# Kernel tuning notes

Hardware: AMD Instinct MI355X
Metric: run time of the kernel (lower is better)

## Reference

```python
import jax, jax.numpy as jnp
import numpy as np

# 27 kernel taps x 3 offset components (dz, dy, dx), matching the module's offset0 list.
OFFSET0 = np.array([
    1, 1, 1, 1, 1, 0, 1, 1, -1, 1, 0, 1, 1, 0, 0, 1, 0, -1, 1, -1, 1, 1, -1, 0, 1, -1, -1,
    0, 1, 1, 0, 1, 0, 0, 1, -1, 0, 0, 1, 0, 0, 0, 0, 0, -1, 0, -1, 1, 0, -1, 0, 0, -1, -1,
    -1, 1, 1, -1, 1, 0, -1, 1, -1, -1, 0, 1, -1, 0, 0, -1, 0, -1, -1, -1, 1, -1, -1, 0, -1, -1, -1
], dtype=np.float64).reshape(27, 3)

BN_EPS = 1e-5


def upsample_nearest2(x):
    # nn.Upsample(scale_factor=2), default mode='nearest', on [B,C,Z,Y,X]
    x = jnp.repeat(x, 2, axis=2)
    x = jnp.repeat(x, 2, axis=3)
    return jnp.repeat(x, 2, axis=4)


def deform_conv3d_static(x, W, b, alpha):
    """3D deformable conv, kernel 3, pad 1, stride 1, with spatially-constant
    per-tap offsets alpha*OFFSET0. Zero padding outside; trilinear sampling.
    Since offsets are static, each tap samples at a fixed fractional shift,
    implemented as a static trilinear combination of slices of the padded input.
    x: [B,C,Z,Y,X], W: [O,C,3,3,3], b: [O].
    """
    B, C, Z, Y, X = x.shape
    # pad 2: 1 for the 3x3x3 kernel + 1 for fractional offsets (|alpha*d| <= 0.7)
    xp = jnp.pad(x, ((0, 0), (0, 0), (2, 2), (2, 2), (2, 2)))
    out = None
    t = 0
    for kz in range(3):
        for ky in range(3):
            for kx in range(3):
                dz, dy, dx = (alpha * OFFSET0[t]).tolist()
                s = (kz - 1 + dz, ky - 1 + dy, kx - 1 + dx)  # shift rel. to output voxel
                f = [int(np.floor(v)) for v in s]
                w = [v - fl for v, fl in zip(s, f)]
                vol = None
                for cz in (0, 1):
                    for cy in (0, 1):
                        for cx in (0, 1):
                            wt = ((w[0] if cz else 1.0 - w[0]) *
                                  (w[1] if cy else 1.0 - w[1]) *
                                  (w[2] if cx else 1.0 - w[2]))
                            if wt == 0.0:
                                continue
                            z0 = 2 + f[0] + cz
                            y0 = 2 + f[1] + cy
                            x0 = 2 + f[2] + cx
                            sl = xp[:, :, z0:z0 + Z, y0:y0 + Y, x0:x0 + X]
                            sl = jnp.float32(wt) * sl
                            vol = sl if vol is None else vol + sl
                contrib = jnp.einsum('oc,bczyx->bozyx', W[:, :, kz, ky, kx], vol)
                out = contrib if out is None else out + contrib
                t += 1
    return out + b[None, :, None, None, None]


def batchnorm(x, g, bt, m, v):
    # eval-mode BatchNorm3d over channel axis 1
    inv = g * jax.lax.rsqrt(v + BN_EPS)
    return x * inv[None, :, None, None, None] + (bt - m * inv)[None, :, None, None, None]


def setup_inputs() -> dict:
    key = jax.random.key(0)
    ks = jax.random.split(key, 13)
    ch_in, ch_out = 64, 32
    x = jax.random.normal(ks[0], (1, ch_in, 32, 32, 32), jnp.float32)
    w_def = jax.random.normal(ks[1], (ch_out, ch_in, 3, 3, 3), jnp.float32) * 0.05
    b_def = jax.random.normal(ks[2], (ch_out,), jnp.float32) * 0.05
    bn1_g = 1.0 + 0.1 * jax.random.normal(ks[3], (ch_out,), jnp.float32)
    bn1_b = 0.1 * jax.random.normal(ks[4], (ch_out,), jnp.float32)
    bn1_m = 0.1 * jax.random.normal(ks[5], (ch_out,), jnp.float32)
    bn1_v = jax.random.uniform(ks[6], (ch_out,), jnp.float32, 0.5, 1.5)
    w_comb = jax.random.normal(ks[7], (ch_out, 3 * ch_out), jnp.float32) * 0.1
    b_comb = 0.05 * jax.random.normal(ks[8], (ch_out,), jnp.float32)
    bn2_g = 1.0 + 0.1 * jax.random.normal(ks[9], (ch_out,), jnp.float32)
    bn2_b = 0.1 * jax.random.normal(ks[10], (ch_out,), jnp.float32)
    bn2_m = 0.1 * jax.random.normal(ks[11], (ch_out,), jnp.float32)
    bn2_v = jax.random.uniform(ks[12], (ch_out,), jnp.float32, 0.5, 1.5)
    return {"x": x, "w_def": w_def, "b_def": b_def,
            "bn1_g": bn1_g, "bn1_b": bn1_b, "bn1_m": bn1_m, "bn1_v": bn1_v,
            "w_comb": w_comb, "b_comb": b_comb,
            "bn2_g": bn2_g, "bn2_b": bn2_b, "bn2_m": bn2_m, "bn2_v": bn2_v}


def reference(x, w_def, b_def, bn1_g, bn1_b, bn1_m, bn1_v,
              w_comb, b_comb, bn2_g, bn2_b, bn2_m, bn2_v):
    xu = upsample_nearest2(x)
    branches = []
    for alpha in (0.0, 0.4, 0.7):  # shared deform-conv weights, three static offset scales
        o = deform_conv3d_static(xu, w_def, b_def, alpha)
        o = jax.nn.relu(batchnorm(o, bn1_g, bn1_b, bn1_m, bn1_v))
        branches.append(o)
    cat = jnp.concatenate(branches, axis=1)  # [B, 3*ch_out, Z,Y,X]
    y = jnp.einsum('oc,bczyx->bozyx', w_comb, cat) + b_comb[None, :, None, None, None]
    y = batchnorm(y, bn2_g, bn2_b, bn2_m, bn2_v)
    return jax.nn.relu(y)
```

## Files before the change

kernel.cpp:

```cpp
#include <hip/hip_runtime.h>


typedef __bf16 bf16x8 __attribute__((ext_vector_type(8)));
typedef float f32x16 __attribute__((ext_vector_type(16)));
typedef unsigned u32x2 __attribute__((ext_vector_type(2)));

__device__ inline unsigned short f2bf(float f) {
  unsigned int u = __float_as_uint(f);
  u += 0x7FFFu + ((u >> 16) & 1u);
  return (unsigned short)(u >> 16);
}

__device__ inline bf16x8 bc16(uint4 v) { return __builtin_bit_cast(bf16x8, v); }

__device__ inline unsigned cvtpk(float lo, float hi) {
  unsigned r;
  asm("v_cvt_pk_bf16_f32 %0, %1, %2" : "=v"(r) : "v"(lo), "v"(hi));
  return r;
}

__device__ inline void plswap(unsigned& a, unsigned& b) {
  u32x2 r = __builtin_amdgcn_permlane32_swap(a, b, false, false);
  a = r.x;
  b = r.y;
}

__device__ inline void gload16(const unsigned short* g, unsigned short* l) {
  __builtin_amdgcn_global_load_lds(
      (const __attribute__((address_space(1))) unsigned int*)(const void*)g,
      (__attribute__((address_space(3))) unsigned int*)(void*)l, 16, 0, 0);
}

__device__ inline float ucoef(int abit, int k, int jbit, float alpha) {
  if (abit == 0) return (k == 0) ? (jbit ? alpha : 1.f - alpha) : (jbit ? 1.f : 0.f);
  return (k == 2) ? (jbit ? 1.f - alpha : alpha) : (jbit ? 0.f : 1.f);
}

#define XREG_USH 524352
#define XZERO_B 1048576u

__global__ void k_prep(const float* __restrict__ x, unsigned short* __restrict__ xT2,
                       const float* __restrict__ w_def, const float* __restrict__ bn1_g,
                       const float* __restrict__ bn1_v, unsigned short* __restrict__ W_sw,
                       const float* __restrict__ w_comb, const float* __restrict__ b_comb,
                       const float* __restrict__ bn2_g, const float* __restrict__ bn2_b,
                       const float* __restrict__ bn2_m, const float* __restrict__ bn2_v,
                       const float* __restrict__ b_def, const float* __restrict__ bn1_b,
                       const float* __restrict__ bn1_m, unsigned short* __restrict__ W2_sw,
                       float* __restrict__ bias1, float* __restrict__ bias2) {
  __shared__ unsigned short t[64][65];
  int bid = blockIdx.x;
  if (bid < 512) {
    int s0 = bid * 64;
    int lane = threadIdx.x & 63;
    int grp = threadIdx.x >> 6;
#pragma unroll
    for (int c = grp; c < 64; c += 4)
      t[c][lane] = f2bf(x[c * 32768 + s0 + lane]);
    __syncthreads();
    int q = lane >> 4, e = lane & 15;
#pragma unroll
    for (int s = grp; s < 64; s += 4)
      xT2[q * XREG_USH + (size_t)(s0 + s) * 16 + e] = t[lane][s];
  } else if (bid < 2048) {
    int e = (bid - 512) * 256 + threadIdx.x;
    int j = e & 7;
    int lane = (e >> 3) & 63;
    int idx = e >> 9;
    int nt = idx % 3;
    idx /= 3;
    int s = idx & 31;
    int p = idx >> 5;
    int o = lane & 31;
    int br = nt;
    int kk = 16 * s + ((lane >> 5) << 3) + j;
    int tap = kk >> 6, ch = kk & 63;
    int jz = (tap >> 2) & 1, jy = (tap >> 1) & 1, jx = tap & 1;
    int a = (p >> 2) & 1, b = (p >> 1) & 1, cp = p & 1;
    float alpha = (br == 0) ? 0.f : ((br == 1) ? 0.4f : 0.7f);
    const float* wb = w_def + (o * 64 + ch) * 27;
    float sum = 0.f;
    for (int kz = 0; kz < 3; ++kz) {
      float uz = ucoef(a, kz, jz, alpha);
      if (uz == 0.f) continue;
      for (int ky = 0; ky < 3; ++ky) {
        float uy = ucoef(b, ky, jy, alpha);
        if (uy == 0.f) continue;
        float uzy = uz * uy;
        for (int kx = 0; kx < 3; ++kx) {
          float ux = ucoef(cp, kx, jx, alpha);
          if (ux != 0.f) sum += wb[kz * 9 + ky * 3 + kx] * uzy * ux;
        }
      }
    }
    float s1 = bn1_g[o] * rsqrtf(bn1_v[o] + 1e-5f);
    W_sw[e] = f2bf(sum * s1);
  } else {
    int tid = threadIdx.x;
    for (int e = tid; e < 3072; e += 256) {
      int j = e & 7;
      int lane = (e >> 3) & 63;
      int s2 = e >> 9;
      int n = lane & 31;
      int k = 16 * s2 + ((lane >> 5) << 3) + j;
      float sc2 = bn2_g[n] * rsqrtf(bn2_v[n] + 1e-5f);
      W2_sw[e] = f2bf(w_comb[n * 96 + k] * sc2);
    }
    {
      int q = tid >> 6, e2 = tid & 63;
      xT2[q * XREG_USH + 524288 + e2] = 0;
    }
    if (tid < 32) {
      float s1 = bn1_g[tid] * rsqrtf(bn1_v[tid] + 1e-5f);
      bias1[tid] = (b_def[tid] - bn1_m[tid]) * s1 + bn1_b[tid];
      float s2 = bn2_g[tid] * rsqrtf(bn2_v[tid] + 1e-5f);
      bias2[tid] = (b_comb[tid] - bn2_m[tid]) * s2 + bn2_b[tid];
    }
  }
}

__launch_bounds__(256, 2)
__global__ void k_main(const unsigned short* __restrict__ xT2,
                       const unsigned short* __restrict__ W_sw,
                       const unsigned short* __restrict__ W2_sw,
                       const float* __restrict__ bias1f,
                       const float* __restrict__ bias2f,
                       float* __restrict__ out) {
  __shared__ unsigned short wring[2][12288];
  __shared__ float blds[64];
  int tid = threadIdx.x;
  int lane = tid & 63;
  int wv = tid >> 6;
  int bid = blockIdx.x;
  int tb = (bid & 7) | ((bid >> 5) << 3);
  int ph = (bid >> 3) & 3;
  int bph = ph & 1, a = ph >> 1;
  int tx = tb & 3, ty = (tb >> 2) & 3, tz = tb >> 4;
  int i0 = tz * 4, j0 = ty * 8, k0 = tx * 8;

  if (tid < 32) {
    blds[tid] = bias1f[tid];
    blds[32 + tid] = bias2f[tid];
  }

  int h = lane >> 5;
  int m = lane & 31;
  int ax = m & 7, ay = (m >> 3) & 1, az = m >> 4;
  int p0 = (a << 2) | (bph << 1);
  unsigned hb = (unsigned)(h << 4);

  const char* xq0 = (const char*)xT2;
  const char* xq1 = xq0 + 1048704;
  const char* xq2 = xq0 + 2097408;
  const char* xq3 = xq0 + 3146112;

  auto stage = [&](int cc) {
    int pn = p0 | (cc >> 2);
    const unsigned short* g =
        W_sw + pn * 49152 + (cc & 3) * 12288 + wv * 3072 + lane * 8;
    unsigned short* l = &wring[cc & 1][wv * 3072];
#pragma unroll
    for (int k = 0; k < 6; ++k) gload16(g + k * 512, l + k * 512);
  };

  __syncthreads();
  stage(0);

  f32x16 osv0, osv1;
  f32x16 acc[2][3];
#pragma unroll
  for (int mt = 0; mt < 2; ++mt)
#pragma unroll
    for (int nt = 0; nt < 3; ++nt) acc[mt][nt] = (f32x16)0.f;

  for (int cc = 0; cc < 8; ++cc) {
    asm volatile("s_waitcnt vmcnt(0)" ::: "memory");
    __builtin_amdgcn_s_barrier();
    __builtin_amdgcn_sched_barrier(0);
    if (cc < 7) stage(cc + 1);
    __builtin_amdgcn_sched_barrier(0);

    int cp = cc >> 2, jy = cc & 1, jz = (cc >> 1) & 1;
    int gz0i = i0 + a - 1 + az + jz;
    int gz1i = gz0i + 2;
    int gyi = j0 + bph - 1 + 2 * wv + ay + jy;
    int gx0i = k0 - 1 + ax + cp;
    int gx1i = gx0i + 1;
    bool oky = (unsigned)gyi < 32u;
    bool okz0 = (unsigned)gz0i < 32u, okz1 = (unsigned)gz1i < 32u;
    bool okx0 = (unsigned)gx0i < 32u, okx1 = (unsigned)gx1i < 32u;
    unsigned s00 = (unsigned)(((gz0i * 32 + gyi) * 32 + gx0i) * 32) + hb;
    unsigned s01 = (unsigned)(((gz1i * 32 + gyi) * 32 + gx0i) * 32) + hb;
    unsigned s10 = (unsigned)(((gz0i * 32 + gyi) * 32 + gx1i) * 32) + hb;
    unsigned s11 = (unsigned)(((gz1i * 32 + gyi) * 32 + gx1i) * 32) + hb;
    unsigned v00 = (oky && okz0 && okx0) ? s00 : XZERO_B;
    unsigned v01 = (oky && okz1 && okx0) ? s01 : XZERO_B;
    unsigned v10 = (oky && okz0 && okx1) ? s10 : XZERO_B;
    unsigned v11 = (oky && okz1 && okx1) ? s11 : XZERO_B;

    const unsigned short* wfb = &wring[cc & 1][lane * 8];
#pragma unroll
    for (int tl = 0; tl < 2; ++tl) {
      unsigned va0 = tl ? v10 : v00;
      unsigned va1 = tl ? v11 : v01;
#pragma unroll
      for (int q = 0; q < 4; ++q) {
        const char* xb = (q == 0) ? xq0 : (q == 1) ? xq1 : (q == 2) ? xq2 : xq3;
        bf16x8 a0 = bc16(*(const uint4*)(xb + va0));
        bf16x8 a1 = bc16(*(const uint4*)(xb + va1));
        const unsigned short* wf = wfb + tl * 6144 + q * 1536;
        bf16x8 bb0 = bc16(*(const uint4*)(wf));
        bf16x8 bb1 = bc16(*(const uint4*)(wf + 512));
        bf16x8 bb2 = bc16(*(const uint4*)(wf + 1024));
        __builtin_amdgcn_s_setprio(1);
        acc[0][0] = __builtin_amdgcn_mfma_f32_32x32x16_bf16(bb0, a0, acc[0][0], 0, 0, 0);
        acc[1][0] = __builtin_amdgcn_mfma_f32_32x32x16_bf16(bb0, a1, acc[1][0], 0, 0, 0);
        acc[0][1] = __builtin_amdgcn_mfma_f32_32x32x16_bf16(bb1, a0, acc[0][1], 0, 0, 0);
        acc[1][1] = __builtin_amdgcn_mfma_f32_32x32x16_bf16(bb1, a1, acc[1][1], 0, 0, 0);
        acc[0][2] = __builtin_amdgcn_mfma_f32_32x32x16_bf16(bb2, a0, acc[0][2], 0, 0, 0);
        acc[1][2] = __builtin_amdgcn_mfma_f32_32x32x16_bf16(bb2, a1, acc[1][2], 0, 0, 0);
        __builtin_amdgcn_s_setprio(0);
      }
    }

    if (cc == 3) {
      const uint4* w2q = (const uint4*)W2_sw;
#pragma unroll
      for (int mt = 0; mt < 2; ++mt) {
        uint4 fr[6];
#pragma unroll
        for (int nt = 0; nt < 3; ++nt) {
          unsigned ww[8];
#pragma unroll
          for (int qc = 0; qc < 8; ++qc) {
            int q = qc >> 1, c2 = qc & 1;
            int r0 = 4 * q + 2 * c2;
            int row = (r0 & 3) + ((r0 >> 2) << 3) + (h << 2);
            float lo = fmaxf(acc[mt][nt][r0] + blds[row], 0.f);
            float hi = fmaxf(acc[mt][nt][r0 + 1] + blds[row + 1], 0.f);
            ww[2 * q + c2] = cvtpk(lo, hi);
          }
          plswap(ww[0], ww[2]);
          plswap(ww[1], ww[3]);
          plswap(ww[4], ww[6]);
          plswap(ww[5], ww[7]);
          fr[2 * nt] = make_uint4(ww[0], ww[1], ww[2], ww[3]);
          fr[2 * nt + 1] = make_uint4(ww[4], ww[5], ww[6], ww[7]);
        }
        f32x16 acc2 = (f32x16)0.f;
#pragma unroll
        for (int s2 = 0; s2 < 6; ++s2)
          acc2 = __builtin_amdgcn_mfma_f32_32x32x16_bf16(bc16(w2q[s2 * 64 + lane]),
                                                         bc16(fr[s2]), acc2, 0, 0, 0);
        f32x16 ov;
#pragma unroll
        for (int r = 0; r < 16; ++r) {
          int row = (r & 3) + ((r >> 2) << 3) + (h << 2);
          ov[r] = fmaxf(acc2[r] + blds[32 + row], 0.f);
        }
        if (mt == 0) osv0 = ov; else osv1 = ov;
#pragma unroll
        for (int nt = 0; nt < 3; ++nt) acc[mt][nt] = (f32x16)0.f;
      }
    }
  }

  {
    const uint4* w2q = (const uint4*)W2_sw;
#pragma unroll
    for (int mt = 0; mt < 2; ++mt) {
      uint4 fr[6];
#pragma unroll
      for (int nt = 0; nt < 3; ++nt) {
        unsigned ww[8];
#pragma unroll
        for (int qc = 0; qc < 8; ++qc) {
          int q = qc >> 1, c2 = qc & 1;
          int r0 = 4 * q + 2 * c2;
          int row = (r0 & 3) + ((r0 >> 2) << 3) + (h << 2);
          float lo = fmaxf(acc[mt][nt][r0] + blds[row], 0.f);
          float hi = fmaxf(acc[mt][nt][r0 + 1] + blds[row + 1], 0.f);
          ww[2 * q + c2] = cvtpk(lo, hi);
        }
        plswap(ww[0], ww[2]);
        plswap(ww[1], ww[3]);
        plswap(ww[4], ww[6]);
        plswap(ww[5], ww[7]);
        fr[2 * nt] = make_uint4(ww[0], ww[1], ww[2], ww[3]);
        fr[2 * nt + 1] = make_uint4(ww[4], ww[5], ww[6], ww[7]);
      }
      f32x16 acc2 = (f32x16)0.f;
#pragma unroll
      for (int s2 = 0; s2 < 6; ++s2)
        acc2 = __builtin_amdgcn_mfma_f32_32x32x16_bf16(bc16(w2q[s2 * 64 + lane]),
                                                       bc16(fr[s2]), acc2, 0, 0, 0);
      f32x16 prev = (mt == 0) ? osv0 : osv1;
      int Z = 2 * (i0 + 2 * mt + az) + a;
      int Y = 2 * (j0 + 2 * wv + ay) + bph;
      float2* o2 = (float2*)out;
#pragma unroll
      for (int r = 0; r < 16; ++r) {
        int ch = (r & 3) + ((r >> 2) << 3) + (h << 2);
        float v1 = fmaxf(acc2[r] + blds[32 + ch], 0.f);
        o2[((size_t)ch << 17) + ((size_t)Z << 11) + (Y << 5) + (k0 + ax)] =
            make_float2(prev[r], v1);
      }
    }
  }
}

extern "C" void kernel_launch(void* const* d_in, const int* in_sizes, int n_in,
                              void* d_out, int out_size, void* d_ws, size_t ws_size,
                              hipStream_t stream) {
  (void)in_sizes; (void)n_in; (void)out_size; (void)ws_size;
  const float* x      = (const float*)d_in[0];
  const float* w_def  = (const float*)d_in[1];
  const float* b_def  = (const float*)d_in[2];
  const float* bn1_g  = (const float*)d_in[3];
  const float* bn1_b  = (const float*)d_in[4];
  const float* bn1_m  = (const float*)d_in[5];
  const float* bn1_v  = (const float*)d_in[6];
  const float* w_comb = (const float*)d_in[7];
  const float* b_comb = (const float*)d_in[8];
  const float* bn2_g  = (const float*)d_in[9];
  const float* bn2_b  = (const float*)d_in[10];
  const float* bn2_m  = (const float*)d_in[11];
  const float* bn2_v  = (const float*)d_in[12];

  char* ws = (char*)d_ws;
  unsigned short* xT2  = (unsigned short*)(ws);
  unsigned short* W_sw = (unsigned short*)(ws + 4194816);
  unsigned short* W2sw = (unsigned short*)(ws + 4981248);
  float* bias1 = (float*)(ws + 4987392);
  float* bias2 = (float*)(ws + 4987520);
  float* out = (float*)d_out;

  hipLaunchKernelGGL(k_prep, dim3(2049), dim3(256), 0, stream,
                     x, xT2, w_def, bn1_g, bn1_v, W_sw,
                     w_comb, b_comb, bn2_g, bn2_b, bn2_m, bn2_v,
                     b_def, bn1_b, bn1_m, W2sw, bias1, bias2);
  hipLaunchKernelGGL(k_main, dim3(512), dim3(256), 0, stream,
                     xT2, W_sw, W2sw, bias1, bias2, out);
}
```

Baseline: 53.74 us.

## Switch main GEMM to 16x16x32 MFMA tiles with smaller spatial tiles and more blocks

Replaces the 32x32x16 MFMA formulation with 16x16x32 bf16 MFMAs. The weight swizzle and the second-stage weight permutation are rebuilt so the first GEMM's accumulator layout feeds the 1x1 combine GEMM directly, which removes the permlane32 swaps. Spatial tiles are halved in y, the grid doubles to 1024 blocks, and launch bounds rise to 3 blocks per CU. The aim is better occupancy and fewer accumulator registers. The cost is more blocks each re-staging the weights, plus a risk of register pressure from the tighter bound.

Result: no change. 54.12 us (+0.7%).

```diff
diff --git a/kernel.cpp b/kernel.cpp
--- a/kernel.cpp
+++ b/kernel.cpp
@@ -2,8 +2,7 @@
 
 
 typedef __bf16 bf16x8 __attribute__((ext_vector_type(8)));
-typedef float f32x16 __attribute__((ext_vector_type(16)));
-typedef unsigned u32x2 __attribute__((ext_vector_type(2)));
+typedef float f32x4 __attribute__((ext_vector_type(4)));
 
 __device__ inline unsigned short f2bf(float f) {
   unsigned int u = __float_as_uint(f);
@@ -17,12 +16,6 @@
   unsigned r;
   asm("v_cvt_pk_bf16_f32 %0, %1, %2" : "=v"(r) : "v"(lo), "v"(hi));
   return r;
-}
-
-__device__ inline void plswap(unsigned& a, unsigned& b) {
-  u32x2 r = __builtin_amdgcn_permlane32_swap(a, b, false, false);
-  a = r.x;
-  b = r.y;
 }
 
 __device__ inline void gload16(const unsigned short* g, unsigned short* l) {
@@ -67,14 +60,14 @@
     int j = e & 7;
     int lane = (e >> 3) & 63;
     int idx = e >> 9;
-    int nt = idx % 3;
-    idx /= 3;
-    int s = idx & 31;
-    int p = idx >> 5;
-    int o = lane & 31;
-    int br = nt;
-    int kk = 16 * s + ((lane >> 5) << 3) + j;
-    int tap = kk >> 6, ch = kk & 63;
+    int ntile = idx % 6;
+    int idx2 = idx / 6;
+    int kstep = idx2 & 15;
+    int p = idx2 >> 4;
+    int n = ntile * 16 + (lane & 15);
+    int o = n & 31, br = n >> 5;
+    int k = (kstep << 5) + ((lane >> 4) << 3) + j;
+    int tap = k >> 6, ch = k & 63;
     int jz = (tap >> 2) & 1, jy = (tap >> 1) & 1, jx = tap & 1;
     int a = (p >> 2) & 1, b = (p >> 1) & 1, cp = p & 1;
     float alpha = (br == 0) ? 0.f : ((br == 1) ? 0.4f : 0.7f);
@@ -100,11 +93,13 @@
     for (int e = tid; e < 3072; e += 256) {
       int j = e & 7;
       int lane = (e >> 3) & 63;
-      int s2 = e >> 9;
-      int n = lane & 31;
-      int k = 16 * s2 + ((lane >> 5) << 3) + j;
-      float sc2 = bn2_g[n] * rsqrtf(bn2_v[n] + 1e-5f);
-      W2_sw[e] = f2bf(w_comb[n * 96 + k] * sc2);
+      int idx = e >> 9;
+      int ks2 = idx % 3, n2t = idx / 3;
+      int n2 = n2t * 16 + (lane & 15);
+      int k2 = (ks2 << 5) + ((lane >> 4) << 3) + j;
+      int pch = (2 * (k2 >> 5) + ((k2 & 7) >> 2)) * 16 + 4 * ((k2 & 31) >> 3) + (k2 & 3);
+      float sc2 = bn2_g[n2] * rsqrtf(bn2_v[n2] + 1e-5f);
+      W2_sw[e] = f2bf(w_comb[n2 * 96 + pch] * sc2);
     }
     {
       int q = tid >> 6, e2 = tid & 63;
@@ -119,7 +114,7 @@
   }
 }
 
-__launch_bounds__(256, 2)
+__launch_bounds__(256, 3)
 __global__ void k_main(const unsigned short* __restrict__ xT2,
                        const unsigned short* __restrict__ W_sw,
                        const unsigned short* __restrict__ W2_sw,
@@ -127,7 +122,7 @@
                        const float* __restrict__ bias2f,
                        float* __restrict__ out) {
   __shared__ unsigned short wring[2][12288];
-  __shared__ float blds[64];
+  __shared__ float blds[128];
   int tid = threadIdx.x;
   int lane = tid & 63;
   int wv = tid >> 6;
@@ -135,24 +130,16 @@
   int tb = (bid & 7) | ((bid >> 5) << 3);
   int ph = (bid >> 3) & 3;
   int bph = ph & 1, a = ph >> 1;
-  int tx = tb & 3, ty = (tb >> 2) & 3, tz = tb >> 4;
-  int i0 = tz * 4, j0 = ty * 8, k0 = tx * 8;
-
-  if (tid < 32) {
-    blds[tid] = bias1f[tid];
-    blds[32 + tid] = bias2f[tid];
-  }
-
-  int h = lane >> 5;
-  int m = lane & 31;
-  int ax = m & 7, ay = (m >> 3) & 1, az = m >> 4;
+  int tx = tb & 3, ty = (tb >> 2) & 7, tz = tb >> 5;
+  int i0 = tz * 4, j0 = ty * 4, k0 = tx * 8;
+
+  if (tid < 96) blds[tid] = bias1f[tid & 31];
+  else if (tid < 128) blds[tid] = bias2f[tid - 96];
+
+  int m = lane & 15, hi = lane >> 4;
+  int ax = m & 7, ay = m >> 3;
   int p0 = (a << 2) | (bph << 1);
-  unsigned hb = (unsigned)(h << 4);
-
-  const char* xq0 = (const char*)xT2;
-  const char* xq1 = xq0 + 1048704;
-  const char* xq2 = xq0 + 2097408;
-  const char* xq3 = xq0 + 3146112;
+  const char* xb0 = (const char*)xT2 + (size_t)(hi >> 1) * 1048704 + ((hi & 1) << 4);
 
   auto stage = [&](int cc) {
     int pn = p0 | (cc >> 2);
@@ -166,12 +153,16 @@
   __syncthreads();
   stage(0);
 
-  f32x16 osv0, osv1;
-  f32x16 acc[2][3];
+  const f32x4* b1v = (const f32x4*)blds;
+  const f32x4* b2v = (const f32x4*)(blds + 96);
+  const uint4* w2q = (const uint4*)W2_sw;
+
+  f32x4 osv[2][2];
+  f32x4 acc[2][6];
 #pragma unroll
   for (int mt = 0; mt < 2; ++mt)
 #pragma unroll
-    for (int nt = 0; nt < 3; ++nt) acc[mt][nt] = (f32x16)0.f;
+    for (int nt = 0; nt < 6; ++nt) acc[mt][nt] = (f32x4)0.f;
 
   for (int cc = 0; cc < 8; ++cc) {
     asm volatile("s_waitcnt vmcnt(0)" ::: "memory");
@@ -180,131 +171,120 @@
     if (cc < 7) stage(cc + 1);
     __builtin_amdgcn_sched_barrier(0);
 
-    int cp = cc >> 2, jy = cc & 1, jz = (cc >> 1) & 1;
-    int gz0i = i0 + a - 1 + az + jz;
-    int gz1i = gz0i + 2;
-    int gyi = j0 + bph - 1 + 2 * wv + ay + jy;
-    int gx0i = k0 - 1 + ax + cp;
-    int gx1i = gx0i + 1;
-    bool oky = (unsigned)gyi < 32u;
-    bool okz0 = (unsigned)gz0i < 32u, okz1 = (unsigned)gz1i < 32u;
-    bool okx0 = (unsigned)gx0i < 32u, okx1 = (unsigned)gx1i < 32u;
-    unsigned s00 = (unsigned)(((gz0i * 32 + gyi) * 32 + gx0i) * 32) + hb;
-    unsigned s01 = (unsigned)(((gz1i * 32 + gyi) * 32 + gx0i) * 32) + hb;
-    unsigned s10 = (unsigned)(((gz0i * 32 + gyi) * 32 + gx1i) * 32) + hb;
-    unsigned s11 = (unsigned)(((gz1i * 32 + gyi) * 32 + gx1i) * 32) + hb;
-    unsigned v00 = (oky && okz0 && okx0) ? s00 : XZERO_B;
-    unsigned v01 = (oky && okz1 && okx0) ? s01 : XZERO_B;
-    unsigned v10 = (oky && okz0 && okx1) ? s10 : XZERO_B;
-    unsigned v11 = (oky && okz1 && okx1) ? s11 : XZERO_B;
-
-    const unsigned short* wfb = &wring[cc & 1][lane * 8];
+    int cp = cc >> 2;
+    unsigned xoff[2][2];
 #pragma unroll
     for (int tl = 0; tl < 2; ++tl) {
-      unsigned va0 = tl ? v10 : v00;
-      unsigned va1 = tl ? v11 : v01;
-#pragma unroll
-      for (int q = 0; q < 4; ++q) {
-        const char* xb = (q == 0) ? xq0 : (q == 1) ? xq1 : (q == 2) ? xq2 : xq3;
-        bf16x8 a0 = bc16(*(const uint4*)(xb + va0));
-        bf16x8 a1 = bc16(*(const uint4*)(xb + va1));
-        const unsigned short* wf = wfb + tl * 6144 + q * 1536;
-        bf16x8 bb0 = bc16(*(const uint4*)(wf));
-        bf16x8 bb1 = bc16(*(const uint4*)(wf + 512));
-        bf16x8 bb2 = bc16(*(const uint4*)(wf + 1024));
-        __builtin_amdgcn_s_setprio(1);
-        acc[0][0] = __builtin_amdgcn_mfma_f32_32x32x16_bf16(bb0, a0, acc[0][0], 0, 0, 0);
-        acc[1][0] = __builtin_amdgcn_mfma_f32_32x32x16_bf16(bb0, a1, acc[1][0], 0, 0, 0);
-        acc[0][1] = __builtin_amdgcn_mfma_f32_32x32x16_bf16(bb1, a0, acc[0][1], 0, 0, 0);
-        acc[1][1] = __builtin_amdgcn_mfma_f32_32x32x16_bf16(bb1, a1, acc[1][1], 0, 0, 0);
-        acc[0][2] = __builtin_amdgcn_mfma_f32_32x32x16_bf16(bb2, a0, acc[0][2], 0, 0, 0);
-        acc[1][2] = __builtin_amdgcn_mfma_f32_32x32x16_bf16(bb2, a1, acc[1][2], 0, 0, 0);
-        __builtin_amdgcn_s_setprio(0);
+      int tap = 2 * (cc & 3) + tl;
+      int jz = (tap >> 2) & 1, jy = (tap >> 1) & 1, jx = tap & 1;
+      int gz = i0 + wv + a - 1 + jz;
+      int gx = k0 + ax + cp - 1 + jx;
+#pragma unroll
+      for (int mt = 0; mt < 2; ++mt) {
+        int gy = j0 + 2 * mt + ay + bph - 1 + jy;
+        bool ok = ((unsigned)gz < 32u) && ((unsigned)gy < 32u) && ((unsigned)gx < 32u);
+        unsigned off = (unsigned)(((gz * 32 + gy) * 32 + gx) * 32);
+        xoff[tl][mt] = ok ? off : XZERO_B;
       }
     }
 
+    const unsigned short* wcb = &wring[cc & 1][lane * 8];
+#pragma unroll
+    for (int ksl = 0; ksl < 4; ++ksl) {
+      int tl = ksl >> 1, khalf = ksl & 1;
+      const char* xp = xb0 + khalf * 2097408;
+      bf16x8 x0 = bc16(*(const uint4*)(xp + xoff[tl][0]));
+      bf16x8 x1 = bc16(*(const uint4*)(xp + xoff[tl][1]));
+      const unsigned short* wk = wcb + ksl * 3072;
+      bf16x8 w0 = bc16(*(const uint4*)(wk));
+      bf16x8 w1 = bc16(*(const uint4*)(wk + 512));
+      bf16x8 w2 = bc16(*(const uint4*)(wk + 1024));
+      bf16x8 w3 = bc16(*(const uint4*)(wk + 1536));
+      bf16x8 w4 = bc16(*(const uint4*)(wk + 2048));
+      bf16x8 w5 = bc16(*(const uint4*)(wk + 2560));
+      __builtin_amdgcn_s_setprio(1);
+      acc[0][0] = __builtin_amdgcn_mfma_f32_16x16x32_bf16(w0, x0, acc[0][0], 0, 0, 0);
+      acc[1][0] = __builtin_amdgcn_mfma_f32_16x16x32_bf16(w0, x1, acc[1][0], 0, 0, 0);
+      acc[0][1] = __builtin_amdgcn_mfma_f32_16x16x32_bf16(w1, x0, acc[0][1], 0, 0, 0);
+      acc[1][1] = __builtin_amdgcn_mfma_f32_16x16x32_bf16(w1, x1, acc[1][1], 0, 0, 0);
+      acc[0][2] = __builtin_amdgcn_mfma_f32_16x16x32_bf16(w2, x0, acc[0][2], 0, 0, 0);
+      acc[1][2] = __builtin_amdgcn_mfma_f32_16x16x32_bf16(w2, x1, acc[1][2], 0, 0, 0);
+      acc[0][3] = __builtin_amdgcn_mfma_f32_16x16x32_bf16(w3, x0, acc[0][3], 0, 0, 0);
+      acc[1][3] = __builtin_amdgcn_mfma_f32_16x16x32_bf16(w3, x1, acc[1][3], 0, 0, 0);
+      acc[0][4] = __builtin_amdgcn_mfma_f32_16x16x32_bf16(w4, x0, acc[0][4], 0, 0, 0);
+      acc[1][4] = __builtin_amdgcn_mfma_f32_16x16x32_bf16(w4, x1, acc[1][4], 0, 0, 0);
+      acc[0][5] = __builtin_amdgcn_mfma_f32_16x16x32_bf16(w5, x0, acc[0][5], 0, 0, 0);
+      acc[1][5] = __builtin_amdgcn_mfma_f32_16x16x32_bf16(w5, x1, acc[1][5], 0, 0, 0);
+      __builtin_amdgcn_s_setprio(0);
+    }
+
     if (cc == 3) {
-      const uint4* w2q = (const uint4*)W2_sw;
 #pragma unroll
       for (int mt = 0; mt < 2; ++mt) {
-        uint4 fr[6];
-#pragma unroll
-        for (int nt = 0; nt < 3; ++nt) {
-          unsigned ww[8];
-#pragma unroll
-          for (int qc = 0; qc < 8; ++qc) {
-            int q = qc >> 1, c2 = qc & 1;
-            int r0 = 4 * q + 2 * c2;
-            int row = (r0 & 3) + ((r0 >> 2) << 3) + (h << 2);
-            float lo = fmaxf(acc[mt][nt][r0] + blds[row], 0.f);
-            float hi = fmaxf(acc[mt][nt][r0 + 1] + blds[row + 1], 0.f);
-            ww[2 * q + c2] = cvtpk(lo, hi);
-          }
-          plswap(ww[0], ww[2]);
-          plswap(ww[1], ww[3]);
-          plswap(ww[4], ww[6]);
-          plswap(ww[5], ww[7]);
-          fr[2 * nt] = make_uint4(ww[0], ww[1], ww[2], ww[3]);
-          fr[2 * nt + 1] = make_uint4(ww[4], ww[5], ww[6], ww[7]);
+        uint4 fr[3];
+#pragma unroll
+        for (int ks2 = 0; ks2 < 3; ++ks2) {
+          f32x4 vA = acc[mt][2 * ks2], vB = acc[mt][2 * ks2 + 1];
+          f32x4 bA = b1v[(2 * ks2) * 4 + hi], bB = b1v[(2 * ks2 + 1) * 4 + hi];
+          fr[ks2] = make_uint4(
+              cvtpk(fmaxf(vA[0] + bA[0], 0.f), fmaxf(vA[1] + bA[1], 0.f)),
+              cvtpk(fmaxf(vA[2] + bA[2], 0.f), fmaxf(vA[3] + bA[3], 0.f)),
+              cvtpk(fmaxf(vB[0] + bB[0], 0.f), fmaxf(vB[1] + bB[1], 0.f)),
+              cvtpk(fmaxf(vB[2] + bB[2], 0.f), fmaxf(vB[3] + bB[3], 0.f)));
         }
-        f32x16 acc2 = (f32x16)0.f;
-#pragma unroll
-        for (int s2 = 0; s2 < 6; ++s2)
-          acc2 = __builtin_amdgcn_mfma_f32_32x32x16_bf16(bc16(w2q[s2 * 64 + lane]),
-                                                         bc16(fr[s2]), acc2, 0, 0, 0);
-        f32x16 ov;
-#pragma unroll
-        for (int r = 0; r < 16; ++r) {
-          int row = (r & 3) + ((r >> 2) << 3) + (h << 2);
-          ov[r] = fmaxf(acc2[r] + blds[32 + row], 0.f);
+        f32x4 a20 = (f32x4)0.f, a21 = (f32x4)0.f;
+#pragma unroll
+        for (int ks2 = 0; ks2 < 3; ++ks2) {
+          a20 = __builtin_amdgcn_mfma_f32_16x16x32_bf16(bc16(w2q[ks2 * 64 + lane]),
+                                                        bc16(fr[ks2]), a20, 0, 0, 0);
+          a21 = __builtin_amdgcn_mfma_f32_16x16x32_bf16(bc16(w2q[(3 + ks2) * 64 + lane]),
+                                                        bc16(fr[ks2]), a21, 0, 0, 0);
         }
-        if (mt == 0) osv0 = ov; else osv1 = ov;
-#pragma unroll
-        for (int nt = 0; nt < 3; ++nt) acc[mt][nt] = (f32x16)0.f;
+        f32x4 b20 = b2v[hi], b21 = b2v[4 + hi];
+#pragma unroll
+        for (int r = 0; r < 4; ++r) {
+          osv[mt][0][r] = fmaxf(a20[r] + b20[r], 0.f);
+          osv[mt][1][r] = fmaxf(a21[r] + b21[r], 0.f);
+        }
+#pragma unroll
+        for (int nt = 0; nt < 6; ++nt) acc[mt][nt] = (f32x4)0.f;
       }
     }
   }
 
-  {
-    const uint4* w2q = (const uint4*)W2_sw;
-#pragma unroll
-    for (int mt = 0; mt < 2; ++mt) {
-      uint4 fr[6];
-#pragma unroll
-      for (int nt = 0; nt < 3; ++nt) {
-        unsigned ww[8];
-#pragma unroll
-        for (int qc = 0; qc < 8; ++qc) {
-          int q = qc >> 1, c2 = qc & 1;
-          int r0 = 4 * q + 2 * c2;
-          int row = (r0 & 3) + ((r0 >> 2) << 3) + (h << 2);
-          float lo = fmaxf(acc[mt][nt][r0] + blds[row], 0.f);
-          float hi = fmaxf(acc[mt][nt][r0 + 1] + blds[row + 1], 0.f);
-          ww[2 * q + c2] = cvtpk(lo, hi);
-        }
-        plswap(ww[0], ww[2]);
-        plswap(ww[1], ww[3]);
-        plswap(ww[4], ww[6]);
-        plswap(ww[5], ww[7]);
-        fr[2 * nt] = make_uint4(ww[0], ww[1], ww[2], ww[3]);
-        fr[2 * nt + 1] = make_uint4(ww[4], ww[5], ww[6], ww[7]);
-      }
-      f32x16 acc2 = (f32x16)0.f;
-#pragma unroll
-      for (int s2 = 0; s2 < 6; ++s2)
-        acc2 = __builtin_amdgcn_mfma_f32_32x32x16_bf16(bc16(w2q[s2 * 64 + lane]),
-                                                       bc16(fr[s2]), acc2, 0, 0, 0);
-      f32x16 prev = (mt == 0) ? osv0 : osv1;
-      int Z = 2 * (i0 + 2 * mt + az) + a;
-      int Y = 2 * (j0 + 2 * wv + ay) + bph;
-      float2* o2 = (float2*)out;
-#pragma unroll
-      for (int r = 0; r < 16; ++r) {
-        int ch = (r & 3) + ((r >> 2) << 3) + (h << 2);
-        float v1 = fmaxf(acc2[r] + blds[32 + ch], 0.f);
-        o2[((size_t)ch << 17) + ((size_t)Z << 11) + (Y << 5) + (k0 + ax)] =
-            make_float2(prev[r], v1);
-      }
+#pragma unroll
+  for (int mt = 0; mt < 2; ++mt) {
+    uint4 fr[3];
+#pragma unroll
+    for (int ks2 = 0; ks2 < 3; ++ks2) {
+      f32x4 vA = acc[mt][2 * ks2], vB = acc[mt][2 * ks2 + 1];
+      f32x4 bA = b1v[(2 * ks2) * 4 + hi], bB = b1v[(2 * ks2 + 1) * 4 + hi];
+      fr[ks2] = make_uint4(
+          cvtpk(fmaxf(vA[0] + bA[0], 0.f), fmaxf(vA[1] + bA[1], 0.f)),
+          cvtpk(fmaxf(vA[2] + bA[2], 0.f), fmaxf(vA[3] + bA[3], 0.f)),
+          cvtpk(fmaxf(vB[0] + bB[0], 0.f), fmaxf(vB[1] + bB[1], 0.f)),
+          cvtpk(fmaxf(vB[2] + bB[2], 0.f), fmaxf(vB[3] + bB[3], 0.f)));
+    }
+    f32x4 a20 = (f32x4)0.f, a21 = (f32x4)0.f;
+#pragma unroll
+    for (int ks2 = 0; ks2 < 3; ++ks2) {
+      a20 = __builtin_amdgcn_mfma_f32_16x16x32_bf16(bc16(w2q[ks2 * 64 + lane]),
+                                                    bc16(fr[ks2]), a20, 0, 0, 0);
+      a21 = __builtin_amdgcn_mfma_f32_16x16x32_bf16(bc16(w2q[(3 + ks2) * 64 + lane]),
+                                                    bc16(fr[ks2]), a21, 0, 0, 0);
+    }
+    f32x4 b20 = b2v[hi], b21 = b2v[4 + hi];
+    int Z = 2 * (i0 + wv) + a;
+    int Y = 2 * (j0 + 2 * mt + ay) + bph;
+    size_t sb = ((size_t)Z << 11) + (Y << 5) + (k0 + ax);
+    float2* o2 = (float2*)out;
+#pragma unroll
+    for (int r = 0; r < 4; ++r) {
+      int ch0 = 4 * hi + r, ch1 = 16 + 4 * hi + r;
+      o2[((size_t)ch0 << 17) + sb] =
+          make_float2(osv[mt][0][r], fmaxf(a20[r] + b20[r], 0.f));
+      o2[((size_t)ch1 << 17) + sb] =
+          make_float2(osv[mt][1][r], fmaxf(a21[r] + b21[r], 0.f));
     }
   }
 }
@@ -339,6 +319,6 @@
                      x, xT2, w_def, bn1_g, bn1_v, W_sw,
                      w_comb, b_comb, bn2_g, bn2_b, bn2_m, bn2_v,
                      b_def, bn1_b, bn1_m, W2sw, bias1, bias2);
-  hipLaunchKernelGGL(k_main, dim3(512), dim3(256), 0, stream,
+  hipLaunchKernelGGL(k_main, dim3(1024), dim3(256), 0, stream,
                      xT2, W_sw, W2sw, bias1, bias2, out);
 }
```

## Split main kernel into 128-thread blocks with per-tap weight staging

Applied to the files above, without the earlier changes.

The main kernel is repartitioned from 512 blocks of 256 threads into 1024 blocks of 128 threads, with launch bounds raised to 3 blocks per CU. Each block covers half the Y extent and walks 16 single-tap iterations instead of 8 two-tap ones, which halves the LDS weight ring. The saved first-phase outputs are now held as packed bf16 instead of fp32 vectors to cut register pressure. The aim is higher occupancy and better latency hiding. The cost is that each weight slice is fetched by twice as many blocks, there are more barriers, and the saved outputs lose precision.

Result: slower. 58.08 us (+8.1%).

```diff
diff --git a/kernel.cpp b/kernel.cpp
--- a/kernel.cpp
+++ b/kernel.cpp
@@ -37,6 +37,7 @@
 }
 
 #define XREG_USH 524352
+#define XREG_B 1048704
 #define XZERO_B 1048576u
 
 __global__ void k_prep(const float* __restrict__ x, unsigned short* __restrict__ xT2,
@@ -119,14 +120,14 @@
   }
 }
 
-__launch_bounds__(256, 2)
+__launch_bounds__(128, 3)
 __global__ void k_main(const unsigned short* __restrict__ xT2,
                        const unsigned short* __restrict__ W_sw,
                        const unsigned short* __restrict__ W2_sw,
                        const float* __restrict__ bias1f,
                        const float* __restrict__ bias2f,
                        float* __restrict__ out) {
-  __shared__ unsigned short wring[2][12288];
+  __shared__ unsigned short wring[2][6144];
   __shared__ float blds[64];
   int tid = threadIdx.x;
   int lane = tid & 63;
@@ -135,30 +136,25 @@
   int tb = (bid & 7) | ((bid >> 5) << 3);
   int ph = (bid >> 3) & 3;
   int bph = ph & 1, a = ph >> 1;
-  int tx = tb & 3, ty = (tb >> 2) & 3, tz = tb >> 4;
-  int i0 = tz * 4, j0 = ty * 8, k0 = tx * 8;
+  int tx = tb & 3, ty = (tb >> 2) & 7, tz = tb >> 5;
+  int i0 = tz * 4, j0 = ty * 4, k0 = tx * 8;
 
   if (tid < 32) {
     blds[tid] = bias1f[tid];
     blds[32 + tid] = bias2f[tid];
   }
 
-  int h = lane >> 5;
-  int m = lane & 31;
-  int ax = m & 7, ay = (m >> 3) & 1, az = m >> 4;
+  int m = lane & 31, h = lane >> 5;
+  int ax = m & 7, ay = (m >> 3) & 1, az = (m >> 4) & 1;
   int p0 = (a << 2) | (bph << 1);
-  unsigned hb = (unsigned)(h << 4);
-
-  const char* xq0 = (const char*)xT2;
-  const char* xq1 = xq0 + 1048704;
-  const char* xq2 = xq0 + 2097408;
-  const char* xq3 = xq0 + 3146112;
-
-  auto stage = [&](int cc) {
-    int pn = p0 | (cc >> 2);
+  int zbase = i0 + 2 * wv + az;
+  const char* xb0 = (const char*)xT2 + (h << 4);
+
+  auto stage = [&](int c) {
+    int pn = p0 | (c >> 3);
     const unsigned short* g =
-        W_sw + pn * 49152 + (cc & 3) * 12288 + wv * 3072 + lane * 8;
-    unsigned short* l = &wring[cc & 1][wv * 3072];
+        W_sw + pn * 49152 + (c & 7) * 6144 + wv * 3072 + lane * 8;
+    unsigned short* l = &wring[c & 1][wv * 3072];
 #pragma unroll
     for (int k = 0; k < 6; ++k) gload16(g + k * 512, l + k * 512);
   };
@@ -166,68 +162,60 @@
   __syncthreads();
   stage(0);
 
-  f32x16 osv0, osv1;
+  unsigned osvp[2][8];
   f32x16 acc[2][3];
 #pragma unroll
   for (int mt = 0; mt < 2; ++mt)
 #pragma unroll
     for (int nt = 0; nt < 3; ++nt) acc[mt][nt] = (f32x16)0.f;
 
-  for (int cc = 0; cc < 8; ++cc) {
+  const uint4* w2q = (const uint4*)W2_sw + lane;
+
+  for (int c = 0; c < 16; ++c) {
     asm volatile("s_waitcnt vmcnt(0)" ::: "memory");
     __builtin_amdgcn_s_barrier();
     __builtin_amdgcn_sched_barrier(0);
-    if (cc < 7) stage(cc + 1);
+    if (c < 15) stage(c + 1);
     __builtin_amdgcn_sched_barrier(0);
 
-    int cp = cc >> 2, jy = cc & 1, jz = (cc >> 1) & 1;
-    int gz0i = i0 + a - 1 + az + jz;
-    int gz1i = gz0i + 2;
-    int gyi = j0 + bph - 1 + 2 * wv + ay + jy;
-    int gx0i = k0 - 1 + ax + cp;
-    int gx1i = gx0i + 1;
-    bool oky = (unsigned)gyi < 32u;
-    bool okz0 = (unsigned)gz0i < 32u, okz1 = (unsigned)gz1i < 32u;
-    bool okx0 = (unsigned)gx0i < 32u, okx1 = (unsigned)gx1i < 32u;
-    unsigned s00 = (unsigned)(((gz0i * 32 + gyi) * 32 + gx0i) * 32) + hb;
-    unsigned s01 = (unsigned)(((gz1i * 32 + gyi) * 32 + gx0i) * 32) + hb;
-    unsigned s10 = (unsigned)(((gz0i * 32 + gyi) * 32 + gx1i) * 32) + hb;
-    unsigned s11 = (unsigned)(((gz1i * 32 + gyi) * 32 + gx1i) * 32) + hb;
-    unsigned v00 = (oky && okz0 && okx0) ? s00 : XZERO_B;
-    unsigned v01 = (oky && okz1 && okx0) ? s01 : XZERO_B;
-    unsigned v10 = (oky && okz0 && okx1) ? s10 : XZERO_B;
-    unsigned v11 = (oky && okz1 && okx1) ? s11 : XZERO_B;
-
-    const unsigned short* wfb = &wring[cc & 1][lane * 8];
-#pragma unroll
-    for (int tl = 0; tl < 2; ++tl) {
-      unsigned va0 = tl ? v10 : v00;
-      unsigned va1 = tl ? v11 : v01;
-#pragma unroll
-      for (int q = 0; q < 4; ++q) {
-        const char* xb = (q == 0) ? xq0 : (q == 1) ? xq1 : (q == 2) ? xq2 : xq3;
-        bf16x8 a0 = bc16(*(const uint4*)(xb + va0));
-        bf16x8 a1 = bc16(*(const uint4*)(xb + va1));
-        const unsigned short* wf = wfb + tl * 6144 + q * 1536;
-        bf16x8 bb0 = bc16(*(const uint4*)(wf));
-        bf16x8 bb1 = bc16(*(const uint4*)(wf + 512));
-        bf16x8 bb2 = bc16(*(const uint4*)(wf + 1024));
-        __builtin_amdgcn_s_setprio(1);
-        acc[0][0] = __builtin_amdgcn_mfma_f32_32x32x16_bf16(bb0, a0, acc[0][0], 0, 0, 0);
-        acc[1][0] = __builtin_amdgcn_mfma_f32_32x32x16_bf16(bb0, a1, acc[1][0], 0, 0, 0);
-        acc[0][1] = __builtin_amdgcn_mfma_f32_32x32x16_bf16(bb1, a0, acc[0][1], 0, 0, 0);
-        acc[1][1] = __builtin_amdgcn_mfma_f32_32x32x16_bf16(bb1, a1, acc[1][1], 0, 0, 0);
-        acc[0][2] = __builtin_amdgcn_mfma_f32_32x32x16_bf16(bb2, a0, acc[0][2], 0, 0, 0);
-        acc[1][2] = __builtin_amdgcn_mfma_f32_32x32x16_bf16(bb2, a1, acc[1][2], 0, 0, 0);
-        __builtin_amdgcn_s_setprio(0);
-      }
-    }
-
-    if (cc == 3) {
-      const uint4* w2q = (const uint4*)W2_sw;
+    int cp = c >> 3, tap = c & 7;
+    int jz = (tap >> 2) & 1, jy = (tap >> 1) & 1, jx = tap & 1;
+    int gz = zbase + a - 1 + jz;
+    int gx = k0 + ax + cp - 1 + jx;
+    bool okzx = ((unsigned)gz < 32u) && ((unsigned)gx < 32u);
+    unsigned xo[2];
+#pragma unroll
+    for (int mt = 0; mt < 2; ++mt) {
+      int gy = j0 + 2 * mt + ay + bph - 1 + jy;
+      bool ok = okzx && ((unsigned)gy < 32u);
+      unsigned off = (unsigned)(((gz * 32 + gy) * 32 + gx) * 32);
+      xo[mt] = ok ? off : XZERO_B;
+    }
+
+    const unsigned short* wfb = &wring[c & 1][lane * 8];
+#pragma unroll
+    for (int q = 0; q < 4; ++q) {
+      const char* xp = xb0 + q * XREG_B;
+      bf16x8 a0 = bc16(*(const uint4*)(xp + xo[0]));
+      bf16x8 a1 = bc16(*(const uint4*)(xp + xo[1]));
+      const unsigned short* wf = wfb + q * 1536;
+      bf16x8 bb0 = bc16(*(const uint4*)(wf));
+      bf16x8 bb1 = bc16(*(const uint4*)(wf + 512));
+      bf16x8 bb2 = bc16(*(const uint4*)(wf + 1024));
+      __builtin_amdgcn_s_setprio(1);
+      acc[0][0] = __builtin_amdgcn_mfma_f32_32x32x16_bf16(bb0, a0, acc[0][0], 0, 0, 0);
+      acc[1][0] = __builtin_amdgcn_mfma_f32_32x32x16_bf16(bb0, a1, acc[1][0], 0, 0, 0);
+      acc[0][1] = __builtin_amdgcn_mfma_f32_32x32x16_bf16(bb1, a0, acc[0][1], 0, 0, 0);
+      acc[1][1] = __builtin_amdgcn_mfma_f32_32x32x16_bf16(bb1, a1, acc[1][1], 0, 0, 0);
+      acc[0][2] = __builtin_amdgcn_mfma_f32_32x32x16_bf16(bb2, a0, acc[0][2], 0, 0, 0);
+      acc[1][2] = __builtin_amdgcn_mfma_f32_32x32x16_bf16(bb2, a1, acc[1][2], 0, 0, 0);
+      __builtin_amdgcn_s_setprio(0);
+    }
+
+    if (c == 7) {
 #pragma unroll
       for (int mt = 0; mt < 2; ++mt) {
-        uint4 fr[6];
+        f32x16 acc2 = (f32x16)0.f;
 #pragma unroll
         for (int nt = 0; nt < 3; ++nt) {
           unsigned ww[8];
@@ -244,67 +232,64 @@
           plswap(ww[1], ww[3]);
           plswap(ww[4], ww[6]);
           plswap(ww[5], ww[7]);
-          fr[2 * nt] = make_uint4(ww[0], ww[1], ww[2], ww[3]);
-          fr[2 * nt + 1] = make_uint4(ww[4], ww[5], ww[6], ww[7]);
+          uint4 frA = make_uint4(ww[0], ww[1], ww[2], ww[3]);
+          uint4 frB = make_uint4(ww[4], ww[5], ww[6], ww[7]);
+          acc2 = __builtin_amdgcn_mfma_f32_32x32x16_bf16(bc16(w2q[(2 * nt) * 64]),
+                                                         bc16(frA), acc2, 0, 0, 0);
+          acc2 = __builtin_amdgcn_mfma_f32_32x32x16_bf16(bc16(w2q[(2 * nt + 1) * 64]),
+                                                         bc16(frB), acc2, 0, 0, 0);
         }
-        f32x16 acc2 = (f32x16)0.f;
-#pragma unroll
-        for (int s2 = 0; s2 < 6; ++s2)
-          acc2 = __builtin_amdgcn_mfma_f32_32x32x16_bf16(bc16(w2q[s2 * 64 + lane]),
-                                                         bc16(fr[s2]), acc2, 0, 0, 0);
-        f32x16 ov;
-#pragma unroll
-        for (int r = 0; r < 16; ++r) {
-          int row = (r & 3) + ((r >> 2) << 3) + (h << 2);
-          ov[r] = fmaxf(acc2[r] + blds[32 + row], 0.f);
+#pragma unroll
+        for (int w = 0; w < 8; ++w) {
+          int r0 = 2 * w;
+          int row = (r0 & 3) + ((r0 >> 2) << 3) + (h << 2);
+          float o0 = fmaxf(acc2[r0] + blds[32 + row], 0.f);
+          float o1 = fmaxf(acc2[r0 + 1] + blds[32 + row + 1], 0.f);
+          osvp[mt][w] = cvtpk(o0, o1);
         }
-        if (mt == 0) osv0 = ov; else osv1 = ov;
 #pragma unroll
         for (int nt = 0; nt < 3; ++nt) acc[mt][nt] = (f32x16)0.f;
       }
     }
   }
 
-  {
-    const uint4* w2q = (const uint4*)W2_sw;
-#pragma unroll
-    for (int mt = 0; mt < 2; ++mt) {
-      uint4 fr[6];
-#pragma unroll
-      for (int nt = 0; nt < 3; ++nt) {
-        unsigned ww[8];
-#pragma unroll
-        for (int qc = 0; qc < 8; ++qc) {
-          int q = qc >> 1, c2 = qc & 1;
-          int r0 = 4 * q + 2 * c2;
-          int row = (r0 & 3) + ((r0 >> 2) << 3) + (h << 2);
-          float lo = fmaxf(acc[mt][nt][r0] + blds[row], 0.f);
-          float hi = fmaxf(acc[mt][nt][r0 + 1] + blds[row + 1], 0.f);
-          ww[2 * q + c2] = cvtpk(lo, hi);
-        }
-        plswap(ww[0], ww[2]);
-        plswap(ww[1], ww[3]);
-        plswap(ww[4], ww[6]);
-        plswap(ww[5], ww[7]);
-        fr[2 * nt] = make_uint4(ww[0], ww[1], ww[2], ww[3]);
-        fr[2 * nt + 1] = make_uint4(ww[4], ww[5], ww[6], ww[7]);
+#pragma unroll
+  for (int mt = 0; mt < 2; ++mt) {
+    f32x16 acc2 = (f32x16)0.f;
+#pragma unroll
+    for (int nt = 0; nt < 3; ++nt) {
+      unsigned ww[8];
+#pragma unroll
+      for (int qc = 0; qc < 8; ++qc) {
+        int q = qc >> 1, c2 = qc & 1;
+        int r0 = 4 * q + 2 * c2;
+        int row = (r0 & 3) + ((r0 >> 2) << 3) + (h << 2);
+        float lo = fmaxf(acc[mt][nt][r0] + blds[row], 0.f);
+        float hi = fmaxf(acc[mt][nt][r0 + 1] + blds[row + 1], 0.f);
+        ww[2 * q + c2] = cvtpk(lo, hi);
       }
-      f32x16 acc2 = (f32x16)0.f;
-#pragma unroll
-      for (int s2 = 0; s2 < 6; ++s2)
-        acc2 = __builtin_amdgcn_mfma_f32_32x32x16_bf16(bc16(w2q[s2 * 64 + lane]),
-                                                       bc16(fr[s2]), acc2, 0, 0, 0);
-      f32x16 prev = (mt == 0) ? osv0 : osv1;
-      int Z = 2 * (i0 + 2 * mt + az) + a;
-      int Y = 2 * (j0 + 2 * wv + ay) + bph;
-      float2* o2 = (float2*)out;
-#pragma unroll
-      for (int r = 0; r < 16; ++r) {
-        int ch = (r & 3) + ((r >> 2) << 3) + (h << 2);
-        float v1 = fmaxf(acc2[r] + blds[32 + ch], 0.f);
-        o2[((size_t)ch << 17) + ((size_t)Z << 11) + (Y << 5) + (k0 + ax)] =
-            make_float2(prev[r], v1);
-      }
+      plswap(ww[0], ww[2]);
+      plswap(ww[1], ww[3]);
+      plswap(ww[4], ww[6]);
+      plswap(ww[5], ww[7]);
+      uint4 frA = make_uint4(ww[0], ww[1], ww[2], ww[3]);
+      uint4 frB = make_uint4(ww[4], ww[5], ww[6], ww[7]);
+      acc2 = __builtin_amdgcn_mfma_f32_32x32x16_bf16(bc16(w2q[(2 * nt) * 64]),
+                                                     bc16(frA), acc2, 0, 0, 0);
+      acc2 = __builtin_amdgcn_mfma_f32_32x32x16_bf16(bc16(w2q[(2 * nt + 1) * 64]),
+                                                     bc16(frB), acc2, 0, 0, 0);
+    }
+    int Z = 2 * zbase + a;
+    int Y = 2 * (j0 + 2 * mt + ay) + bph;
+    size_t sb = ((size_t)Z << 11) + (Y << 5) + (k0 + ax);
+    float2* o2 = (float2*)out;
+#pragma unroll
+    for (int r = 0; r < 16; ++r) {
+      int ch = (r & 3) + ((r >> 2) << 3) + (h << 2);
+      float v1 = fmaxf(acc2[r] + blds[32 + ch], 0.f);
+      unsigned pw = osvp[mt][r >> 1];
+      float pv = __uint_as_float((r & 1) ? (pw & 0xffff0000u) : (pw << 16));
+      o2[((size_t)ch << 17) + sb] = make_float2(pv, v1);
     }
   }
 }
@@ -339,6 +324,6 @@
                      x, xT2, w_def, bn1_g, bn1_v, W_sw,
                      w_comb, b_comb, bn2_g, bn2_b, bn2_m, bn2_v,
                      b_def, bn1_b, bn1_m, W2sw, bias1, bias2);
-  hipLaunchKernelGGL(k_main, dim3(512), dim3(256), 0, stream,
+  hipLaunchKernelGGL(k_main, dim3(1024), dim3(128), 0, stream,
                      xT2, W_sw, W2sw, bias1, bias2, out);
 }
```
